# Kernel tuning notes

Hardware: AMD Instinct MI355X
Metric: run time of the kernel (lower is better)

## Reference

```python
import jax, jax.numpy as jnp
import numpy as np

PT, SKIP, CNN_UNITS, RNN_UNITS = 16, 32, 512, 512


def setup_inputs() -> dict:
    key = jax.random.key(0)
    k_x, k_w, k_u = jax.random.split(key, 3)
    B, T, C, H = 128, 512, CNN_UNITS, RNN_UNITS
    # 0.05 scaling keeps the relu GRU recurrence numerically stable
    x = jax.random.normal(k_x, (B, T, C), dtype=jnp.float32)
    W = jax.random.normal(k_w, (C, 3 * H), dtype=jnp.float32) * 0.05
    U = jax.random.normal(k_u, (H, 3 * H), dtype=jnp.float32) * 0.05
    b = jnp.zeros((2, 3 * H), dtype=jnp.float32)  # [input_bias, recurrent_bias] (reset_after=True)
    return {"x": x, "W": W, "U": U, "b": b}


def reference(x, W, U, b):
    B, T, C = x.shape
    H = U.shape[0]
    pt, skip = PT, SKIP
    # pretrans: last pt*skip steps -> (B, pt, skip, C) -> (B, skip, pt, C) -> (B*skip, pt, C)
    s = x[:, -pt * skip:, :]
    s = s.reshape(B, pt, skip, C).transpose(0, 2, 1, 3).reshape(B * skip, pt, C)
    # precompute input projections for all timesteps: (pt, B*skip, 3H)
    xp = jnp.einsum('ntc,ch->tnh', s, W) + b[0]
    b_rec = b[1]

    def step(h, xt):
        rec = h @ U + b_rec                      # (N, 3H)
        xz, xr, xh = jnp.split(xt, 3, axis=-1)
        rz, rr, rh = jnp.split(rec, 3, axis=-1)
        z = jax.nn.sigmoid(xz + rz)
        r = jax.nn.sigmoid(xr + rr)
        hh = jax.nn.relu(xh + r * rh)            # activation='relu'
        h_new = z * h + (1.0 - z) * hh
        return h_new, None

    h0 = jnp.zeros((B * skip, H), dtype=x.dtype)
    h_final, _ = jax.lax.scan(step, h0, xp)
    # posttrans: (B*skip, H) -> (B, skip*H)
    return h_final.reshape(B, skip * H)
```

## Files before the change

kernel.cpp:

```cpp
#include <hip/hip_runtime.h>
#include <cstddef>


typedef unsigned short u16;
typedef __attribute__((ext_vector_type(8))) short short8;
typedef __attribute__((ext_vector_type(8))) u16 u16x8;
typedef __attribute__((ext_vector_type(4))) float floatx4;

#define MFMA16(a, b, c) __builtin_amdgcn_mfma_f32_16x16x32_bf16((a), (b), (c), 0, 0, 0)

__device__ __forceinline__ u16 f32_to_bf16(float f) {
  union { float f; unsigned int u; } c; c.f = f;
  unsigned int u = c.u + 0x7FFFu + ((c.u >> 16) & 1u);
  return (u16)(u >> 16);
}
__device__ __forceinline__ float bf16_to_f32(u16 v) {
  union { unsigned int u; float f; } c; c.u = ((unsigned int)v) << 16;
  return c.f;
}
__device__ __forceinline__ float sigmoidf_(float x) {
  return 1.0f / (1.0f + __expf(-x));
}
__device__ __forceinline__ void gload_lds16(const void* g, void* l) {
  __builtin_amdgcn_global_load_lds(
      (const __attribute__((address_space(1))) unsigned int*)g,
      (__attribute__((address_space(3))) unsigned int*)l, 16, 0, 0);
}

__global__ void pack_x(const float* __restrict__ x, u16* __restrict__ xb) {
  size_t gid = (size_t)blockIdx.x * 256 + threadIdx.x;
  int row  = (int)(gid & 63);
  int g    = (int)((gid >> 6) & 3);
  int kt   = (int)((gid >> 8) & 15);
  int nblk = (int)((gid >> 12) & 63);
  int t    = (int)(gid >> 18);
  int n = nblk * 64 + row, b = n >> 5, s = n & 31;
  const float* src = x + ((size_t)(b * 512 + t * 32 + s) * 512 + kt * 32 + g * 8);
  floatx4 va = *(const floatx4*)src;
  floatx4 vb = *(const floatx4*)(src + 4);
  u16x8 pk;
  pk[0] = f32_to_bf16(va[0]); pk[1] = f32_to_bf16(va[1]);
  pk[2] = f32_to_bf16(va[2]); pk[3] = f32_to_bf16(va[3]);
  pk[4] = f32_to_bf16(vb[0]); pk[5] = f32_to_bf16(vb[1]);
  pk[6] = f32_to_bf16(vb[2]); pk[7] = f32_to_bf16(vb[3]);
  *(u16x8*)(xb + gid * 8) = pk;
}

__global__ void pack_Bt(const float* __restrict__ W, const float* __restrict__ U,
                        u16* __restrict__ Bt) {
  size_t gid = (size_t)blockIdx.x * 256 + threadIdx.x;
  int col = (int)(gid & 63);
  int g   = (int)((gid >> 6) & 3);
  int kt  = (int)((gid >> 8) & 31);
  int cc  = (int)(gid >> 13);
  int c = cc * 64 + col;
  int k0 = kt * 32 + g * 8;
  u16x8 pk;
#pragma unroll
  for (int j = 0; j < 8; ++j) {
    int k = k0 + j;
    float v = (k < 512) ? W[(size_t)k * 1536 + c] : U[(size_t)(k - 512) * 1536 + c];
    pk[j] = f32_to_bf16(v);
  }
  *(u16x8*)(Bt + gid * 8) = pk;
}

__global__ __launch_bounds__(256)
void gru_step(const u16* __restrict__ xb, const u16* __restrict__ Bt,
              const float* __restrict__ bias,
              const u16* __restrict__ h_in, u16* __restrict__ h_out,
              float* __restrict__ out, int t, int first, int last) {
  __shared__ alignas(16) char sm[32768];
  const int tid = threadIdx.x;
  const int idx = blockIdx.x;
  const int nb = ((idx >> 6) << 3) | (idx & 7);
  const int hb = (idx >> 3) & 7;
  const int w = tid >> 6;
  const int lane = tid & 63;
  const int wy = w >> 1, wx = w & 1;
  const int q = lane >> 4, lc = lane & 15;

  const u16* xbB = xb + (size_t)(t * 64 + nb) * 32768;
  const u16* htB = h_in + (size_t)nb * 32768;
  const int cs0 = hb, cs1 = 8 + hb, cs2 = 16 + hb;

  floatx4 acZ[2][2] = {{{0.f,0.f,0.f,0.f},{0.f,0.f,0.f,0.f}},{{0.f,0.f,0.f,0.f},{0.f,0.f,0.f,0.f}}};
  floatx4 acR[2][2] = {{{0.f,0.f,0.f,0.f},{0.f,0.f,0.f,0.f}},{{0.f,0.f,0.f,0.f},{0.f,0.f,0.f,0.f}}};
  floatx4 acX[2][2] = {{{0.f,0.f,0.f,0.f},{0.f,0.f,0.f,0.f}},{{0.f,0.f,0.f,0.f},{0.f,0.f,0.f,0.f}}};
  floatx4 acH[2][2] = {{{0.f,0.f,0.f,0.f},{0.f,0.f,0.f,0.f}},{{0.f,0.f,0.f,0.f},{0.f,0.f,0.f,0.f}}};

  const int ktall = first ? 16 : 32;
  const int wo = w * 1024;

  auto stage = [&](int kt, int bsel) {
    char* lds = sm + bsel * 16384;
    const char* aS = (const char*)((kt < 16) ? (xbB + (size_t)kt * 2048)
                                             : (htB + (size_t)(kt - 16) * 2048));
    gload_lds16(aS + wo + lane * 16, lds + wo);
    gload_lds16((const char*)(Bt + (size_t)(cs0 * 32 + kt) * 2048) + wo + lane * 16,
                lds + 4096 + wo);
    gload_lds16((const char*)(Bt + (size_t)(cs1 * 32 + kt) * 2048) + wo + lane * 16,
                lds + 8192 + wo);
    gload_lds16((const char*)(Bt + (size_t)(cs2 * 32 + kt) * 2048) + wo + lane * 16,
                lds + 12288 + wo);
  };

  auto compute = [&](int bsel, floatx4 (&acT)[2][2]) {
    const char* lds = sm + bsel * 16384;
    short8 a0 = *(const short8*)(lds + (q * 64 + wy * 32 + lc) * 16);
    short8 a1 = *(const short8*)(lds + (q * 64 + wy * 32 + 16 + lc) * 16);
#pragma unroll
    for (int ci = 0; ci < 2; ++ci) {
      int co = (q * 64 + wx * 32 + ci * 16 + lc) * 16;
      short8 bz = *(const short8*)(lds + 4096 + co);
      short8 br = *(const short8*)(lds + 8192 + co);
      short8 bh = *(const short8*)(lds + 12288 + co);
      acZ[0][ci] = MFMA16(a0, bz, acZ[0][ci]);
      acZ[1][ci] = MFMA16(a1, bz, acZ[1][ci]);
      acR[0][ci] = MFMA16(a0, br, acR[0][ci]);
      acR[1][ci] = MFMA16(a1, br, acR[1][ci]);
      acT[0][ci] = MFMA16(a0, bh, acT[0][ci]);
      acT[1][ci] = MFMA16(a1, bh, acT[1][ci]);
    }
  };

  stage(0, 0);
  __syncthreads();
  for (int kt = 0; kt < 16; ++kt) {
    if (kt + 1 < ktall) stage(kt + 1, (kt + 1) & 1);
    compute(kt & 1, acX);
    __syncthreads();
  }
  if (!first) {
    for (int kt = 16; kt < 32; ++kt) {
      if (kt + 1 < 32) stage(kt + 1, (kt + 1) & 1);
      compute(kt & 1, acH);
      __syncthreads();
    }
  }

  const float* b0 = bias;
  const float* b1 = bias + 1536;
  u16* Ct = (u16*)sm;
#pragma unroll
  for (int ci = 0; ci < 2; ++ci) {
    const int hcl = wx * 32 + ci * 16 + lc;
    const int hg = hb * 64 + hcl;
    const float bz = b0[hg] + b1[hg];
    const float br = b0[512 + hg] + b1[512 + hg];
    const float b0h = b0[1024 + hg];
    const float b1h = b1[1024 + hg];
    const int ktg = hg >> 5;
    const int gg = (hg >> 3) & 3;
    const size_t hbase = (((size_t)nb * 16 + ktg) * 4 + gg) * 64;
#pragma unroll
    for (int mi = 0; mi < 2; ++mi) {
#pragma unroll
      for (int reg = 0; reg < 4; ++reg) {
        const int nl = wy * 32 + mi * 16 + q * 4 + reg;
        const int n = nb * 64 + nl;
        float z = sigmoidf_(acZ[mi][ci][reg] + bz);
        float r = sigmoidf_(acR[mi][ci][reg] + br);
        float hh = acX[mi][ci][reg] + b0h + r * (acH[mi][ci][reg] + b1h);
        hh = fmaxf(hh, 0.0f);
        float hp = 0.0f;
        if (!first) hp = bf16_to_f32(h_in[(hbase + nl) * 8 + (hg & 7)]);
        float v = z * hp + (1.0f - z) * hh;
        if (last) out[(size_t)n * 512 + hg] = v;
        else      Ct[nl * 72 + hcl] = f32_to_bf16(v);
      }
    }
  }
  if (!last) {
    __syncthreads();
#pragma unroll
    for (int i = 0; i < 2; ++i) {
      int e = i * 256 + tid;
      int row = e & 63;
      int g = (e >> 6) & 3;
      int ktl = e >> 8;
      u16x8 vv = *(const u16x8*)(Ct + row * 72 + ktl * 32 + g * 8);
      *(u16x8*)(h_out + ((((size_t)nb * 16 + (hb * 2 + ktl)) * 4 + g) * 64 + row) * 8) = vv;
    }
  }
}

extern "C" void kernel_launch(void* const* d_in, const int* in_sizes, int n_in,
                              void* d_out, int out_size, void* d_ws, size_t ws_size,
                              hipStream_t stream) {
  const float* x = (const float*)d_in[0];
  const float* W = (const float*)d_in[1];
  const float* U = (const float*)d_in[2];
  const float* bias = (const float*)d_in[3];
  float* out = (float*)d_out;

  u16* xb = (u16*)d_ws;
  u16* Bt = xb + (size_t)16 * 64 * 32768;
  u16* h0 = Bt + (size_t)1536 * 1024;
  u16* h1 = h0 + (size_t)4096 * 512;

  pack_x<<<16384, 256, 0, stream>>>(x, xb);
  pack_Bt<<<768, 256, 0, stream>>>(W, U, Bt);

  for (int t = 0; t < 16; ++t) {
    const u16* hin = (t & 1) ? h1 : h0;
    u16* hout = (t & 1) ? h0 : h1;
    gru_step<<<512, 256, 0, stream>>>(
        xb, Bt, bias, hin, hout, out, t, (t == 0) ? 1 : 0, (t == 15) ? 1 : 0);
  }
}
```

Measured before the change: 558.8 us.

## Retile GRU step to 128-row blocks with 64-wide K chunks; coalesce pack_x via LDS

Each GRU step block now covers 128 batch rows and 32 hidden columns per gate, loading K in 64-element chunks. This halves the number of barriers and raises A-tile reuse across gates. pack_x is rewritten to read contiguous x rows into swizzled shared memory and write the packed bf16 tile contiguously, replacing strided gathers. The cost is larger LDS use (57KB) and a padded output staging stride that may produce unaligned shared-memory vector reads.

```diff
diff --git a/kernel.cpp b/kernel.cpp
--- a/kernel.cpp
+++ b/kernel.cpp
@@ -27,23 +27,37 @@
       (__attribute__((address_space(3))) unsigned int*)l, 16, 0, 0);
 }
 
-__global__ void pack_x(const float* __restrict__ x, u16* __restrict__ xb) {
-  size_t gid = (size_t)blockIdx.x * 256 + threadIdx.x;
-  int row  = (int)(gid & 63);
-  int g    = (int)((gid >> 6) & 3);
-  int kt   = (int)((gid >> 8) & 15);
-  int nblk = (int)((gid >> 12) & 63);
-  int t    = (int)(gid >> 18);
-  int n = nblk * 64 + row, b = n >> 5, s = n & 31;
-  const float* src = x + ((size_t)(b * 512 + t * 32 + s) * 512 + kt * 32 + g * 8);
-  floatx4 va = *(const floatx4*)src;
-  floatx4 vb = *(const floatx4*)(src + 4);
-  u16x8 pk;
-  pk[0] = f32_to_bf16(va[0]); pk[1] = f32_to_bf16(va[1]);
-  pk[2] = f32_to_bf16(va[2]); pk[3] = f32_to_bf16(va[3]);
-  pk[4] = f32_to_bf16(vb[0]); pk[5] = f32_to_bf16(vb[1]);
-  pk[6] = f32_to_bf16(vb[2]); pk[7] = f32_to_bf16(vb[3]);
-  *(u16x8*)(xb + gid * 8) = pk;
+__global__ __launch_bounds__(256)
+void pack_x(const float* __restrict__ x, u16* __restrict__ xb) {
+  __shared__ u16 sm[64 * 512];
+  const int t = blockIdx.x >> 6;
+  const int nb = blockIdx.x & 63;
+  const int tid = threadIdx.x;
+#pragma unroll
+  for (int it = 0; it < 16; ++it) {
+    int idx = it * 256 + tid;
+    int row = idx >> 6, ch = idx & 63;
+    int xrow = (nb * 2 + (row >> 5)) * 512 + t * 32 + (row & 31);
+    const float* src = x + (size_t)xrow * 512 + ch * 8;
+    floatx4 va = *(const floatx4*)src;
+    floatx4 vb = *(const floatx4*)(src + 4);
+    u16x8 pk;
+    pk[0] = f32_to_bf16(va[0]); pk[1] = f32_to_bf16(va[1]);
+    pk[2] = f32_to_bf16(va[2]); pk[3] = f32_to_bf16(va[3]);
+    pk[4] = f32_to_bf16(vb[0]); pk[5] = f32_to_bf16(vb[1]);
+    pk[6] = f32_to_bf16(vb[2]); pk[7] = f32_to_bf16(vb[3]);
+    *(u16x8*)&sm[row * 512 + (ch ^ (row & 7)) * 8] = pk;
+  }
+  __syncthreads();
+  u16* dst = xb + (size_t)blockIdx.x * 32768;
+#pragma unroll
+  for (int it = 0; it < 16; ++it) {
+    int idx = it * 256 + tid;
+    int row = idx & 63, g = (idx >> 6) & 3, kt = idx >> 8;
+    int ch = kt * 4 + g;
+    u16x8 vv = *(const u16x8*)&sm[row * 512 + (ch ^ (row & 7)) * 8];
+    *(u16x8*)(dst + (size_t)idx * 8) = vv;
+  }
 }
 
 __global__ void pack_Bt(const float* __restrict__ W, const float* __restrict__ U,
@@ -65,110 +79,116 @@
   *(u16x8*)(Bt + gid * 8) = pk;
 }
 
-__global__ __launch_bounds__(256)
+__global__ __launch_bounds__(256, 2)
 void gru_step(const u16* __restrict__ xb, const u16* __restrict__ Bt,
               const float* __restrict__ bias,
               const u16* __restrict__ h_in, u16* __restrict__ h_out,
               float* __restrict__ out, int t, int first, int last) {
-  __shared__ alignas(16) char sm[32768];
+  __shared__ alignas(16) char sm[57344];
   const int tid = threadIdx.x;
-  const int idx = blockIdx.x;
-  const int nb = ((idx >> 6) << 3) | (idx & 7);
-  const int hb = (idx >> 3) & 7;
-  const int w = tid >> 6;
-  const int lane = tid & 63;
+  const int nb2 = blockIdx.x & 31;
+  const int hb  = blockIdx.x >> 5;
+  const int w = tid >> 6, lane = tid & 63;
   const int wy = w >> 1, wx = w & 1;
   const int q = lane >> 4, lc = lane & 15;
 
-  const u16* xbB = xb + (size_t)(t * 64 + nb) * 32768;
-  const u16* htB = h_in + (size_t)nb * 32768;
-  const int cs0 = hb, cs1 = 8 + hb, cs2 = 16 + hb;
-
-  floatx4 acZ[2][2] = {{{0.f,0.f,0.f,0.f},{0.f,0.f,0.f,0.f}},{{0.f,0.f,0.f,0.f},{0.f,0.f,0.f,0.f}}};
-  floatx4 acR[2][2] = {{{0.f,0.f,0.f,0.f},{0.f,0.f,0.f,0.f}},{{0.f,0.f,0.f,0.f},{0.f,0.f,0.f,0.f}}};
-  floatx4 acX[2][2] = {{{0.f,0.f,0.f,0.f},{0.f,0.f,0.f,0.f}},{{0.f,0.f,0.f,0.f},{0.f,0.f,0.f,0.f}}};
-  floatx4 acH[2][2] = {{{0.f,0.f,0.f,0.f},{0.f,0.f,0.f,0.f}},{{0.f,0.f,0.f,0.f},{0.f,0.f,0.f,0.f}}};
-
-  const int ktall = first ? 16 : 32;
-  const int wo = w * 1024;
-
-  auto stage = [&](int kt, int bsel) {
-    char* lds = sm + bsel * 16384;
-    const char* aS = (const char*)((kt < 16) ? (xbB + (size_t)kt * 2048)
-                                             : (htB + (size_t)(kt - 16) * 2048));
-    gload_lds16(aS + wo + lane * 16, lds + wo);
-    gload_lds16((const char*)(Bt + (size_t)(cs0 * 32 + kt) * 2048) + wo + lane * 16,
-                lds + 4096 + wo);
-    gload_lds16((const char*)(Bt + (size_t)(cs1 * 32 + kt) * 2048) + wo + lane * 16,
-                lds + 8192 + wo);
-    gload_lds16((const char*)(Bt + (size_t)(cs2 * 32 + kt) * 2048) + wo + lane * 16,
-                lds + 12288 + wo);
+  const char* xA0 = (const char*)(xb + (size_t)(t * 64 + nb2 * 2) * 32768);
+  const char* xA1 = xA0 + 65536;
+  const char* hA0 = (const char*)(h_in + (size_t)(nb2 * 2) * 32768);
+  const char* hA1 = hA0 + 65536;
+  const char* BtB = (const char*)Bt;
+  const int colh = (hb & 1) * 512;
+  const int cc0 = hb >> 1;
+
+  floatx4 acZ[4] = {{0.f,0.f,0.f,0.f},{0.f,0.f,0.f,0.f},{0.f,0.f,0.f,0.f},{0.f,0.f,0.f,0.f}};
+  floatx4 acR[4] = {{0.f,0.f,0.f,0.f},{0.f,0.f,0.f,0.f},{0.f,0.f,0.f,0.f},{0.f,0.f,0.f,0.f}};
+  floatx4 acX[4] = {{0.f,0.f,0.f,0.f},{0.f,0.f,0.f,0.f},{0.f,0.f,0.f,0.f},{0.f,0.f,0.f,0.f}};
+  floatx4 acH[4] = {{0.f,0.f,0.f,0.f},{0.f,0.f,0.f,0.f},{0.f,0.f,0.f,0.f},{0.f,0.f,0.f,0.f}};
+
+  const int nch = first ? 8 : 16;
+
+  auto stage = [&](int kc, int bsel) {
+    char* lds = sm + bsel * 28672;
+#pragma unroll
+    for (int j = 0; j < 7; ++j) {
+      int i = w * 7 + j;
+      if (i < 16) {
+        int sub = i >> 3, ktl = (i >> 2) & 1, qq = i & 3;
+        const char* base =
+            (kc < 8) ? ((sub ? xA1 : xA0) + (size_t)kc * 8192)
+                     : ((sub ? hA1 : hA0) + (size_t)(kc - 8) * 8192);
+        gload_lds16(base + ktl * 4096 + qq * 1024 + lane * 16,
+                    lds + sub * 8192 + ktl * 4096 + qq * 1024);
+      } else {
+        int bi = i - 16;
+        int gate = bi >> 2, ktl = (bi >> 1) & 1, gh = bi & 1;
+        int cc = cc0 + gate * 8;
+        int ktg = kc * 2 + ktl;
+        gload_lds16(BtB + (size_t)(cc * 32 + ktg) * 4096
+                        + (gh * 2 + (lane >> 5)) * 1024 + colh + (lane & 31) * 16,
+                    lds + 16384 + gate * 4096 + ktl * 2048 + gh * 1024);
+      }
+    }
   };
 
-  auto compute = [&](int bsel, floatx4 (&acT)[2][2]) {
-    const char* lds = sm + bsel * 16384;
-    short8 a0 = *(const short8*)(lds + (q * 64 + wy * 32 + lc) * 16);
-    short8 a1 = *(const short8*)(lds + (q * 64 + wy * 32 + 16 + lc) * 16);
-#pragma unroll
-    for (int ci = 0; ci < 2; ++ci) {
-      int co = (q * 64 + wx * 32 + ci * 16 + lc) * 16;
-      short8 bz = *(const short8*)(lds + 4096 + co);
-      short8 br = *(const short8*)(lds + 8192 + co);
-      short8 bh = *(const short8*)(lds + 12288 + co);
-      acZ[0][ci] = MFMA16(a0, bz, acZ[0][ci]);
-      acZ[1][ci] = MFMA16(a1, bz, acZ[1][ci]);
-      acR[0][ci] = MFMA16(a0, br, acR[0][ci]);
-      acR[1][ci] = MFMA16(a1, br, acR[1][ci]);
-      acT[0][ci] = MFMA16(a0, bh, acT[0][ci]);
-      acT[1][ci] = MFMA16(a1, bh, acT[1][ci]);
+  auto compute = [&](int bsel, floatx4 (&acT)[4]) {
+    const char* lds = sm + bsel * 28672;
+#pragma unroll
+    for (int jj = 0; jj < 2; ++jj) {
+      const char* Ab = lds + wy * 8192 + jj * 4096;
+      short8 a0 = *(const short8*)(Ab + (q * 64 +      lc) * 16);
+      short8 a1 = *(const short8*)(Ab + (q * 64 + 16 + lc) * 16);
+      short8 a2 = *(const short8*)(Ab + (q * 64 + 32 + lc) * 16);
+      short8 a3 = *(const short8*)(Ab + (q * 64 + 48 + lc) * 16);
+      const char* Bb = lds + 16384 + jj * 2048;
+      int co = q * 512 + (wx * 16 + lc) * 16;
+      short8 bz = *(const short8*)(Bb + co);
+      short8 br = *(const short8*)(Bb + 4096 + co);
+      short8 bh = *(const short8*)(Bb + 8192 + co);
+      acZ[0] = MFMA16(a0, bz, acZ[0]); acZ[1] = MFMA16(a1, bz, acZ[1]);
+      acZ[2] = MFMA16(a2, bz, acZ[2]); acZ[3] = MFMA16(a3, bz, acZ[3]);
+      acR[0] = MFMA16(a0, br, acR[0]); acR[1] = MFMA16(a1, br, acR[1]);
+      acR[2] = MFMA16(a2, br, acR[2]); acR[3] = MFMA16(a3, br, acR[3]);
+      acT[0] = MFMA16(a0, bh, acT[0]); acT[1] = MFMA16(a1, bh, acT[1]);
+      acT[2] = MFMA16(a2, bh, acT[2]); acT[3] = MFMA16(a3, bh, acT[3]);
     }
   };
 
   stage(0, 0);
   __syncthreads();
-  for (int kt = 0; kt < 16; ++kt) {
-    if (kt + 1 < ktall) stage(kt + 1, (kt + 1) & 1);
-    compute(kt & 1, acX);
+  for (int kc = 0; kc < nch; ++kc) {
+    if (kc + 1 < nch) stage(kc + 1, (kc + 1) & 1);
+    if (kc < 8) compute(kc & 1, acX);
+    else        compute(kc & 1, acH);
     __syncthreads();
-  }
-  if (!first) {
-    for (int kt = 16; kt < 32; ++kt) {
-      if (kt + 1 < 32) stage(kt + 1, (kt + 1) & 1);
-      compute(kt & 1, acH);
-      __syncthreads();
-    }
   }
 
   const float* b0 = bias;
   const float* b1 = bias + 1536;
+  const int hcl = wx * 16 + lc;
+  const int hg = hb * 32 + hcl;
+  const float bz = b0[hg] + b1[hg];
+  const float brr = b0[512 + hg] + b1[512 + hg];
+  const float b0h = b0[1024 + hg];
+  const float b1h = b1[1024 + hg];
+  const int nbw = nb2 * 2 + wy;
   u16* Ct = (u16*)sm;
 #pragma unroll
-  for (int ci = 0; ci < 2; ++ci) {
-    const int hcl = wx * 32 + ci * 16 + lc;
-    const int hg = hb * 64 + hcl;
-    const float bz = b0[hg] + b1[hg];
-    const float br = b0[512 + hg] + b1[512 + hg];
-    const float b0h = b0[1024 + hg];
-    const float b1h = b1[1024 + hg];
-    const int ktg = hg >> 5;
-    const int gg = (hg >> 3) & 3;
-    const size_t hbase = (((size_t)nb * 16 + ktg) * 4 + gg) * 64;
-#pragma unroll
-    for (int mi = 0; mi < 2; ++mi) {
-#pragma unroll
-      for (int reg = 0; reg < 4; ++reg) {
-        const int nl = wy * 32 + mi * 16 + q * 4 + reg;
-        const int n = nb * 64 + nl;
-        float z = sigmoidf_(acZ[mi][ci][reg] + bz);
-        float r = sigmoidf_(acR[mi][ci][reg] + br);
-        float hh = acX[mi][ci][reg] + b0h + r * (acH[mi][ci][reg] + b1h);
-        hh = fmaxf(hh, 0.0f);
-        float hp = 0.0f;
-        if (!first) hp = bf16_to_f32(h_in[(hbase + nl) * 8 + (hg & 7)]);
-        float v = z * hp + (1.0f - z) * hh;
-        if (last) out[(size_t)n * 512 + hg] = v;
-        else      Ct[nl * 72 + hcl] = f32_to_bf16(v);
-      }
+  for (int mi = 0; mi < 4; ++mi) {
+#pragma unroll
+    for (int reg = 0; reg < 4; ++reg) {
+      int nl64 = mi * 16 + q * 4 + reg;
+      float z = sigmoidf_(acZ[mi][reg] + bz);
+      float r = sigmoidf_(acR[mi][reg] + brr);
+      float hh = acX[mi][reg] + b0h + r * (acH[mi][reg] + b1h);
+      hh = fmaxf(hh, 0.0f);
+      float hp = 0.0f;
+      if (!first)
+        hp = bf16_to_f32(h_in[(((size_t)nbw * 16 + hb) * 4 + (hcl >> 3)) * 512
+                              + nl64 * 8 + (hcl & 7)]);
+      float v = z * hp + (1.0f - z) * hh;
+      if (last) out[((size_t)nbw * 64 + nl64) * 512 + hg] = v;
+      else      Ct[(wy * 64 + nl64) * 34 + hcl] = f32_to_bf16(v);
     }
   }
   if (!last) {
@@ -176,11 +196,9 @@
 #pragma unroll
     for (int i = 0; i < 2; ++i) {
       int e = i * 256 + tid;
-      int row = e & 63;
-      int g = (e >> 6) & 3;
-      int ktl = e >> 8;
-      u16x8 vv = *(const u16x8*)(Ct + row * 72 + ktl * 32 + g * 8);
-      *(u16x8*)(h_out + ((((size_t)nb * 16 + (hb * 2 + ktl)) * 4 + g) * 64 + row) * 8) = vv;
+      int row = e & 63, g = (e >> 6) & 3, sub = e >> 8;
+      u16x8 vv = *(const u16x8*)&Ct[(sub * 64 + row) * 34 + g * 8];
+      *(u16x8*)(h_out + ((((size_t)(nb2 * 2 + sub) * 16 + hb) * 4 + g) * 64 + row) * 8) = vv;
     }
   }
 }
@@ -199,7 +217,7 @@
   u16* h0 = Bt + (size_t)1536 * 1024;
   u16* h1 = h0 + (size_t)4096 * 512;
 
-  pack_x<<<16384, 256, 0, stream>>>(x, xb);
+  pack_x<<<1024, 256, 0, stream>>>(x, xb);
   pack_Bt<<<768, 256, 0, stream>>>(W, U, Bt);
 
   for (int t = 0; t < 16; ++t) {
```

After: 1.582 ms. +183.1%, slower.
